# Kernel tuning notes

Measured on AMD Instinct MI355X. Metric: run time of the kernel, lower is better.

## Reference

```python
import jax, jax.numpy as jnp
import numpy as np

B, S, D, H = 4, 2048, 2048, 16
DH = D // H


def setup_inputs() -> dict:
    key = jax.random.key(0)
    ks = jax.random.split(key, 11)
    p = 0.02  # keep pre-softmax logits in a sane range
    return {
        "x": jax.random.normal(ks[0], (B, S, D), jnp.float32),
        "Wq": jax.random.normal(ks[1], (D, D), jnp.float32) * p,
        "bq": jax.random.normal(ks[2], (D,), jnp.float32) * p,
        "Wk": jax.random.normal(ks[3], (D, D), jnp.float32) * p,
        "bk": jax.random.normal(ks[4], (D,), jnp.float32) * p,
        "Wv": jax.random.normal(ks[5], (D, D), jnp.float32) * p,
        "bv": jax.random.normal(ks[6], (D,), jnp.float32) * p,
        "Wo": jax.random.normal(ks[7], (D, D), jnp.float32) * p,
        "bo": jax.random.normal(ks[8], (D,), jnp.float32) * p,
        "spiral_weight": jax.random.normal(ks[9], (H,), jnp.float32),
        "helix_rotation": jax.random.normal(ks[10], (D,), jnp.float32),
    }


def reference(x, Wq, bq, Wk, bk, Wv, bv, Wo, bo, spiral_weight, helix_rotation):
    b, s, d = x.shape
    h, dh = H, d // H
    # projections (torch Linear: x @ W.T + b), split into heads
    q = (x @ Wq.T + bq).reshape(b, s, h, dh)
    k = (x @ Wk.T + bk).reshape(b, s, h, dh)
    v = (x @ Wv.T + bv).reshape(b, s, h, dh)
    # cos/sin helix gating, applied per (head, head_dim) channel
    rot = helix_rotation.reshape(h, dh)
    q = q * jnp.cos(rot)
    k = k * jnp.sin(rot)
    # per-head scaled scores: [b,h,s,s]
    scores = jnp.einsum("bshd,bthd->bhst", q, k) / np.sqrt(dh).astype(np.float32)
    scores = scores * spiral_weight[None, :, None, None]
    attn = jax.nn.softmax(scores, axis=-1)
    out = jnp.einsum("bhst,bthd->bshd", attn, v).reshape(b, s, d)
    return out @ Wo.T + bo
```

## Files before the change

kernel.cpp:

```cpp
#include <hip/hip_runtime.h>
#include <math.h>

#define B_ 4
#define S_ 2048
#define D_ 2048
#define H_ 16
#define DH_ 128

typedef unsigned short u16;
typedef unsigned int u32;
typedef u16 u16x8 __attribute__((ext_vector_type(8)));
typedef __bf16 bf16x8 __attribute__((ext_vector_type(8)));
typedef float f32x4 __attribute__((ext_vector_type(4)));

__device__ inline u16 f2bf(float f) {
    unsigned int u = __builtin_bit_cast(unsigned int, f);
    unsigned int lsb = (u >> 16) & 1u;
    u += 0x7fffu + lsb;
    return (u16)(u >> 16);
}

__device__ inline f32x4 mfma16(u16x8 a, u16x8 b, f32x4 c) {
    return __builtin_amdgcn_mfma_f32_16x16x32_bf16(
        __builtin_bit_cast(bf16x8, a), __builtin_bit_cast(bf16x8, b), c, 0, 0, 0);
}

__device__ inline void gl2lds16(const u16* g, u16* l) {
    __builtin_amdgcn_global_load_lds(
        (const __attribute__((address_space(1))) void*)g,
        (__attribute__((address_space(3))) void*)l, 16, 0, 0);
}

__device__ inline void block_barrier() {
    asm volatile("" ::: "memory");
    __builtin_amdgcn_s_barrier();
    asm volatile("" ::: "memory");
}

__global__ __launch_bounds__(256) void cvt_f32_bf16(const float* __restrict__ src,
                                                    u16* __restrict__ dst, int n8) {
    int i = blockIdx.x * 256 + threadIdx.x;
    if (i >= n8) return;
    const float4* s = (const float4*)src + (size_t)i * 2;
    float4 a = s[0], b = s[1];
    u16x8 o;
    o[0] = f2bf(a.x); o[1] = f2bf(a.y); o[2] = f2bf(a.z); o[3] = f2bf(a.w);
    o[4] = f2bf(b.x); o[5] = f2bf(b.y); o[6] = f2bf(b.z); o[7] = f2bf(b.w);
    *((u16x8*)dst + i) = o;
}

__global__ __launch_bounds__(256) void cvt4_f32_bf16(const float* __restrict__ s0,
                                                     const float* __restrict__ s1,
                                                     const float* __restrict__ s2,
                                                     const float* __restrict__ s3,
                                                     u16* __restrict__ dst) {
    const int region = blockIdx.x >> 11;
    const int i = (blockIdx.x & 2047) * 256 + threadIdx.x;
    const float* src = region == 0 ? s0 : region == 1 ? s1 : region == 2 ? s2 : s3;
    const float4* s = (const float4*)src + (size_t)i * 2;
    float4 a = s[0], b = s[1];
    u16x8 o;
    o[0] = f2bf(a.x); o[1] = f2bf(a.y); o[2] = f2bf(a.z); o[3] = f2bf(a.w);
    o[4] = f2bf(b.x); o[5] = f2bf(b.y); o[6] = f2bf(b.z); o[7] = f2bf(b.w);
    *((u16x8*)dst + (size_t)region * 524288 + i) = o;
}

template <typename OutT>
__device__ __forceinline__ void gemm_core(const u16* __restrict__ A,
                                          const u16* __restrict__ Bw,
                                          const float* __restrict__ bias,
                                          const float* __restrict__ helix,
                                          OutT* __restrict__ C,
                                          int N, int K,
                                          int tm, int tn, int gate, int vout) {
    __shared__ __align__(16) u16 As[2][256 * 64];
    __shared__ __align__(16) u16 Bs[2][256 * 64];

    const int tid = threadIdx.x;
    const int lane = tid & 63, w = tid >> 6;
    const int lr = lane & 15, quad = lane >> 4;
    const int wm = w & 1, wn = w >> 1;
    const int NT = K >> 6;

    const u16* Asrc = A + (size_t)(tm * 256) * K;
    const u16* Bsrc = Bw + (size_t)(tn * 256) * K;

    u32 go[4][2];
    u32 lo[4][2];
#pragma unroll
    for (int q = 0; q < 2; ++q) {
        const int seg = w * 2 + q;
        const int i0 = seg * 8 + (lane >> 3);
        const int s0 = seg * 8;
        int row = (i0 & 63) | ((i0 >> 6) << 7);
        int rb = (s0 & 63) | ((s0 >> 6) << 7);
        go[0][q] = (u32)row * K + (((lane & 7) ^ (row & 7)) << 3);
        lo[0][q] = rb << 6;
        row += 64; rb += 64;
        go[3][q] = (u32)row * K + (((lane & 7) ^ (row & 7)) << 3);
        lo[3][q] = rb << 6;
        row = (i0 & 31) | ((i0 >> 5) << 6);
        rb = (s0 & 31) | ((s0 >> 5) << 6);
        go[1][q] = (u32)row * K + (((lane & 7) ^ (row & 7)) << 3);
        lo[1][q] = rb << 6;
        row += 32; rb += 32;
        go[2][q] = (u32)row * K + (((lane & 7) ^ (row & 7)) << 3);
        lo[2][q] = rb << 6;
    }

#define STAGE(u, tt)                                                          \
    do {                                                                      \
        const int kt_ = (((tt) < NT) ? (tt) : (NT - 1)) << 6;                 \
        const u16* gb_ = ((u) == 1 || (u) == 2) ? Bsrc : Asrc;                \
        u16* lb_ = ((u) == 1 || (u) == 2) ? Bs[(tt) & 1] : As[(tt) & 1];      \
        gl2lds16(gb_ + go[u][0] + kt_, lb_ + lo[u][0]);                       \
        gl2lds16(gb_ + go[u][1] + kt_, lb_ + lo[u][1]);                       \
    } while (0)

    const int koff0 = (quad * 8) ^ ((lr & 7) * 8);
    const int koff1 = (32 + quad * 8) ^ ((lr & 7) * 8);
    const int rA = wm * 128 + lr;
    const int rB = wn * 64 + lr;

    f32x4 zero = {0.f, 0.f, 0.f, 0.f};
    f32x4 acc[8][4];
#pragma unroll
    for (int im = 0; im < 8; ++im)
#pragma unroll
        for (int jn = 0; jn < 4; ++jn) acc[im][jn] = zero;

    u16x8 af[4][2], bf[4][2];

    STAGE(0, 0); STAGE(1, 0); STAGE(2, 0); STAGE(3, 0);
    STAGE(0, 1); STAGE(1, 1); STAGE(2, 1);
    asm volatile("s_waitcnt vmcnt(6)" ::: "memory");
    block_barrier();

    for (int t = 0; t < NT; ++t) {
        const u16* Ab = As[t & 1];
        const u16* Bb = Bs[t & 1];

#pragma unroll
        for (int im = 0; im < 4; ++im) {
            af[im][0] = *(const u16x8*)&Ab[(rA + im * 16) * 64 + koff0];
            af[im][1] = *(const u16x8*)&Ab[(rA + im * 16) * 64 + koff1];
        }
#pragma unroll
        for (int jn = 0; jn < 2; ++jn) {
            bf[jn][0] = *(const u16x8*)&Bb[(rB + jn * 16) * 64 + koff0];
            bf[jn][1] = *(const u16x8*)&Bb[(rB + jn * 16) * 64 + koff1];
        }
        STAGE(3, t + 1);
        block_barrier();
        asm volatile("s_waitcnt lgkmcnt(0)" ::: "memory");
        __builtin_amdgcn_s_setprio(1);
#pragma unroll
        for (int s = 0; s < 2; ++s)
#pragma unroll
            for (int im = 0; im < 4; ++im)
#pragma unroll
                for (int jn = 0; jn < 2; ++jn)
                    acc[im][jn] = mfma16(af[im][s], bf[jn][s], acc[im][jn]);
        __builtin_amdgcn_s_setprio(0);
        block_barrier();

#pragma unroll
        for (int jn = 2; jn < 4; ++jn) {
            bf[jn][0] = *(const u16x8*)&Bb[(rB + jn * 16) * 64 + koff0];
            bf[jn][1] = *(const u16x8*)&Bb[(rB + jn * 16) * 64 + koff1];
        }
        STAGE(0, t + 2);
        block_barrier();
        asm volatile("s_waitcnt lgkmcnt(0)" ::: "memory");
        __builtin_amdgcn_s_setprio(1);
#pragma unroll
        for (int s = 0; s < 2; ++s)
#pragma unroll
            for (int im = 0; im < 4; ++im)
#pragma unroll
                for (int jn = 2; jn < 4; ++jn)
                    acc[im][jn] = mfma16(af[im][s], bf[jn][s], acc[im][jn]);
        __builtin_amdgcn_s_setprio(0);
        block_barrier();

#pragma unroll
        for (int im = 0; im < 4; ++im) {
            af[im][0] = *(const u16x8*)&Ab[(rA + 64 + im * 16) * 64 + koff0];
            af[im][1] = *(const u16x8*)&Ab[(rA + 64 + im * 16) * 64 + koff1];
        }
        STAGE(1, t + 2);
        block_barrier();
        asm volatile("s_waitcnt lgkmcnt(0)" ::: "memory");
        __builtin_amdgcn_s_setprio(1);
#pragma unroll
        for (int s = 0; s < 2; ++s)
#pragma unroll
            for (int im = 0; im < 4; ++im)
#pragma unroll
                for (int jn = 0; jn < 2; ++jn)
                    acc[im + 4][jn] = mfma16(af[im][s], bf[jn][s], acc[im + 4][jn]);
        __builtin_amdgcn_s_setprio(0);
        block_barrier();

        STAGE(2, t + 2);
        asm volatile("s_waitcnt vmcnt(6)" ::: "memory");
        block_barrier();
        __builtin_amdgcn_s_setprio(1);
#pragma unroll
        for (int s = 0; s < 2; ++s)
#pragma unroll
            for (int im = 0; im < 4; ++im)
#pragma unroll
                for (int jn = 2; jn < 4; ++jn)
                    acc[im + 4][jn] = mfma16(af[im][s], bf[jn][s], acc[im + 4][jn]);
        __builtin_amdgcn_s_setprio(0);
        block_barrier();
    }
    asm volatile("s_waitcnt vmcnt(0)" ::: "memory");
#undef STAGE

    if (vout) {
#pragma unroll
        for (int im = 0; im < 8; ++im)
#pragma unroll
            for (int r = 0; r < 4; ++r) {
                int row = tm * 256 + wm * 128 + im * 16 + quad * 4 + r;
                float bs = bias[row];
#pragma unroll
                for (int jn = 0; jn < 4; ++jn) {
                    int col = tn * 256 + wn * 64 + jn * 16 + lr;
                    float val = acc[im][jn][r] + bs;
                    ((u16*)C)[(size_t)(col >> 11) * ((size_t)D_ * S_) +
                              (size_t)row * S_ + (col & (S_ - 1))] = f2bf(val);
                }
            }
    } else {
#pragma unroll
        for (int jn = 0; jn < 4; ++jn) {
            int col = tn * 256 + wn * 64 + jn * 16 + lr;
            float bs = bias[col];
            float g = 1.0f;
            if (gate == 1) g = cosf(helix[col]);
            if (gate == 2) g = sinf(helix[col]);
#pragma unroll
            for (int im = 0; im < 8; ++im)
#pragma unroll
                for (int r = 0; r < 4; ++r) {
                    int row = tm * 256 + wm * 128 + im * 16 + quad * 4 + r;
                    float val = (acc[im][jn][r] + bs) * g;
                    if constexpr (sizeof(OutT) == 2)
                        ((u16*)C)[(size_t)row * N + col] = f2bf(val);
                    else
                        ((float*)C)[(size_t)row * N + col] = val;
                }
        }
    }
}

template <typename OutT>
__global__ __launch_bounds__(512, 2) void gemm256(const u16* __restrict__ A,
                                                  const u16* __restrict__ Bw,
                                                  const float* __restrict__ bias,
                                                  const float* __restrict__ helix,
                                                  OutT* __restrict__ C,
                                                  int N, int K, int gate) {
    gemm_core<OutT>(A, Bw, bias, helix, C, N, K, blockIdx.y, blockIdx.x, gate, 0);
}

__global__ __launch_bounds__(512, 2) void gemm256_qkv(const u16* __restrict__ xbf,
                                                      const u16* __restrict__ Wq,
                                                      const u16* __restrict__ Wk,
                                                      const u16* __restrict__ Wv,
                                                      const float* __restrict__ bq,
                                                      const float* __restrict__ bk,
                                                      const float* __restrict__ bv,
                                                      const float* __restrict__ helix,
                                                      u16* __restrict__ Cq,
                                                      u16* __restrict__ Ck,
                                                      u16* __restrict__ Cv) {
    const int bid = blockIdx.x;
    const int region = bid >> 8;
    const int r = bid & 255;
    const u16* A;
    const u16* Bw;
    const float* bias;
    u16* C;
    int tm, tn, gate, vout;
    if (region == 0) {
        A = xbf; Bw = Wq; bias = bq; C = Cq;
        tn = r & 7; tm = r >> 3; gate = 1; vout = 0;
    } else if (region == 1) {
        A = xbf; Bw = Wk; bias = bk; C = Ck;
        tn = r & 7; tm = r >> 3; gate = 2; vout = 0;
    } else {
        A = Wv; Bw = xbf; bias = bv; C = Cv;
        tn = r & 31; tm = r >> 5; gate = 0; vout = 1;
    }
    gemm_core<u16>(A, Bw, bias, helix, C, D_, D_, tm, tn, gate, vout);
}

__global__ __launch_bounds__(256, 2) void helix_attn(const u16* __restrict__ Q,
                                                     const u16* __restrict__ Kq,
                                                     const u16* __restrict__ Vt,
                                                     const float* __restrict__ spiral,
                                                     u16* __restrict__ O) {
    __shared__ __align__(16) u16 Ks[64 * 128];
    __shared__ __align__(16) u16 Vs[128 * 64];
    __shared__ __align__(16) u16 Ps[128 * 64];

    const int tid = threadIdx.x;
    const int lane = tid & 63, w = tid >> 6;
    const int lr = lane & 15, quad = lane >> 4;

    const int bx = blockIdx.x;
    const int qt = bx & 15;
    const int h = (bx >> 4) & 15;
    const int b = bx >> 8;

    const size_t headoff = (size_t)b * S_ * D_ + (size_t)h * DH_;
    const u16* qp = Q + headoff;
    const u16* kp = Kq + headoff;
    const u16* vtp = Vt + ((size_t)b * H_ + h) * (size_t)DH_ * S_;

    const float scale2 = spiral[h] * 0.08838834764831845f * 1.4426950408889634f;

    u16x8 qf[2][4];
#pragma unroll
    for (int mb = 0; mb < 2; ++mb)
#pragma unroll
        for (int c = 0; c < 4; ++c) {
            u16x8 raw = *(const u16x8*)(qp + (size_t)(qt * 128 + mb * 64 + w * 16 + lr) * D_ +
                                        c * 32 + quad * 8);
#pragma unroll
            for (int j = 0; j < 8; ++j) {
                float f = __builtin_bit_cast(float, (u32)raw[j] << 16) * scale2;
                qf[mb][c][j] = f2bf(f);
            }
        }

    f32x4 zero = {0.f, 0.f, 0.f, 0.f};
    f32x4 Oacc[2][8];
#pragma unroll
    for (int mb = 0; mb < 2; ++mb)
#pragma unroll
        for (int n = 0; n < 8; ++n) Oacc[mb][n] = zero;
    float rs[2][4] = {{0.f, 0.f, 0.f, 0.f}, {0.f, 0.f, 0.f, 0.f}};

    const int rsw = (lr >> 1) & 7;
    const int wsw = (quad * 2) & 7;
    const int ksw = lr & 7;

    for (int tt = 0; tt < 32; ++tt) {
        const int t0 = tt * 64;
        __syncthreads();
#pragma unroll
        for (int p = 0; p < 4; ++p) {
            int lin = p * 256 + tid;
            int trow = lin >> 4;
            int kch = lin & 15;
            *(u16x8*)&Ks[trow * 128 + ((kch ^ (trow & 7)) * 8)] =
                *(const u16x8*)(kp + (size_t)(t0 + trow) * D_ + kch * 8);
            int drow = lin >> 3;
            int lc = lin & 7;
            *(u16x8*)&Vs[drow * 64 + ((lc ^ (drow & 7)) * 8)] =
                *(const u16x8*)(vtp + (size_t)drow * S_ + t0 + lc * 8);
        }
        __syncthreads();

        f32x4 Sacc[2][4] = {{zero, zero, zero, zero}, {zero, zero, zero, zero}};
#pragma unroll
        for (int c = 0; c < 4; ++c) {
#pragma unroll
            for (int j = 0; j < 4; ++j) {
                u16x8 kf = *(const u16x8*)&Ks[(j * 16 + lr) * 128 +
                                              (((c * 4 + quad) ^ ksw) * 8)];
                Sacc[0][j] = mfma16(qf[0][c], kf, Sacc[0][j]);
                Sacc[1][j] = mfma16(qf[1][c], kf, Sacc[1][j]);
            }
        }

#pragma unroll
        for (int mb = 0; mb < 2; ++mb)
#pragma unroll
            for (int j = 0; j < 4; ++j)
#pragma unroll
                for (int r = 0; r < 4; ++r) {
                    float p = exp2f(Sacc[mb][j][r]);
                    u32 u = __builtin_bit_cast(u32, p);
                    rs[mb][r] += __builtin_bit_cast(float, u & 0xffff0000u);
                    int prow = mb * 64 + w * 16 + quad * 4 + r;
                    int pchunk = (j * 2 + (lr >> 3)) ^ ((wsw + (r >> 1)) & 7);
                    Ps[prow * 64 + pchunk * 8 + (lr & 7)] = (u16)(u >> 16);
                }

#pragma unroll
        for (int ks = 0; ks < 2; ++ks) {
            int pch = ((ks * 4 + quad) ^ rsw) * 8;
            u16x8 pf0 = *(const u16x8*)&Ps[(w * 16 + lr) * 64 + pch];
            u16x8 pf1 = *(const u16x8*)&Ps[(64 + w * 16 + lr) * 64 + pch];
#pragma unroll
            for (int n = 0; n < 8; ++n) {
                u16x8 vf = *(const u16x8*)&Vs[(n * 16 + lr) * 64 +
                                              (((ks * 4 + quad) ^ ksw) * 8)];
                Oacc[0][n] = mfma16(pf0, vf, Oacc[0][n]);
                Oacc[1][n] = mfma16(pf1, vf, Oacc[1][n]);
            }
        }
    }

#pragma unroll
    for (int mb = 0; mb < 2; ++mb)
#pragma unroll
        for (int r = 0; r < 4; ++r) {
            float s = rs[mb][r];
#pragma unroll
            for (int off = 1; off < 16; off <<= 1) s += __shfl_xor(s, off, 64);
            float inv = 1.0f / s;
            int row = qt * 128 + mb * 64 + w * 16 + quad * 4 + r;
            u16* op = O + headoff + (size_t)row * D_;
#pragma unroll
            for (int n = 0; n < 8; ++n) op[n * 16 + lr] = f2bf(Oacc[mb][n][r] * inv);
        }
}

extern "C" void kernel_launch(void* const* d_in, const int* in_sizes, int n_in,
                              void* d_out, int out_size, void* d_ws, size_t ws_size,
                              hipStream_t stream) {
    const float* x = (const float*)d_in[0];
    const float* Wq = (const float*)d_in[1];
    const float* bq = (const float*)d_in[2];
    const float* Wk = (const float*)d_in[3];
    const float* bk = (const float*)d_in[4];
    const float* Wv = (const float*)d_in[5];
    const float* bv = (const float*)d_in[6];
    const float* Wo = (const float*)d_in[7];
    const float* bo = (const float*)d_in[8];
    const float* spiral = (const float*)d_in[9];
    const float* helix = (const float*)d_in[10];
    float* out = (float*)d_out;

    char* ws = (char*)d_ws;
    u16* xbf = (u16*)(ws);
    u16* wqb = (u16*)(ws + 33554432);
    u16* wkb = (u16*)(ws + 33554432 + 8388608);
    u16* wvb = (u16*)(ws + 33554432 + 16777216);
    u16* wob = (u16*)(ws + 33554432 + 25165824);
    u16* qb = (u16*)(ws + 67108864);
    u16* kb = (u16*)(ws + 67108864 + 33554432);
    u16* vtb = (u16*)(ws + 67108864 + 67108864);
    u16* attnb = xbf;

    const int NX = B_ * S_ * D_;

    cvt_f32_bf16<<<NX / 8 / 256, 256, 0, stream>>>(x, xbf, NX / 8);
    cvt4_f32_bf16<<<4 * 2048, 256, 0, stream>>>(Wq, Wk, Wv, Wo, wqb);

    gemm256_qkv<<<768, 512, 0, stream>>>(xbf, wqb, wkb, wvb, bq, bk, bv, helix,
                                         qb, kb, vtb);

    helix_attn<<<B_ * H_ * (S_ / 128), 256, 0, stream>>>(qb, kb, vtb, spiral, attnb);

    dim3 gq(D_ / 256, (B_ * S_) / 256);
    gemm256<float><<<gq, 512, 0, stream>>>(attnb, wob, bo, nullptr, out, D_, D_, 0);
}
```

Measured before the change: 691.1 us.

## Switch projection GEMM to 32x32x16 MFMA and pad attention V/P LDS tiles

The shared GEMM core now uses 32x32x16 bf16 MFMA tiles instead of 16x16x32. This halves the number of MFMA issues and changes fragment loads and the epilogue row mapping to match the 32x32 output layout. In the attention kernel, the Vs and Ps LDS buffers move from XOR swizzling to a padded row stride of 72, aiming to cut bank conflicts and address arithmetic. In exchange, the larger accumulator fragments may raise register pressure, the padded buffers use more LDS, and Ps keeps its XOR chunk index alongside the padding.

```diff
diff --git a/kernel.cpp b/kernel.cpp
--- a/kernel.cpp
+++ b/kernel.cpp
@@ -12,6 +12,7 @@
 typedef u16 u16x8 __attribute__((ext_vector_type(8)));
 typedef __bf16 bf16x8 __attribute__((ext_vector_type(8)));
 typedef float f32x4 __attribute__((ext_vector_type(4)));
+typedef float f32x16 __attribute__((ext_vector_type(16)));
 
 __device__ inline u16 f2bf(float f) {
     unsigned int u = __builtin_bit_cast(unsigned int, f);
@@ -22,6 +23,11 @@
 
 __device__ inline f32x4 mfma16(u16x8 a, u16x8 b, f32x4 c) {
     return __builtin_amdgcn_mfma_f32_16x16x32_bf16(
+        __builtin_bit_cast(bf16x8, a), __builtin_bit_cast(bf16x8, b), c, 0, 0, 0);
+}
+
+__device__ inline f32x16 mfma32(u16x8 a, u16x8 b, f32x16 c) {
+    return __builtin_amdgcn_mfma_f32_32x32x16_bf16(
         __builtin_bit_cast(bf16x8, a), __builtin_bit_cast(bf16x8, b), c, 0, 0, 0);
 }
 
@@ -78,7 +84,7 @@
 
     const int tid = threadIdx.x;
     const int lane = tid & 63, w = tid >> 6;
-    const int lr = lane & 15, quad = lane >> 4;
+    const int r32 = lane & 31, hi = lane >> 5;
     const int wm = w & 1, wn = w >> 1;
     const int NT = K >> 6;
 
@@ -117,19 +123,21 @@
         gl2lds16(gb_ + go[u][1] + kt_, lb_ + lo[u][1]);                       \
     } while (0)
 
-    const int koff0 = (quad * 8) ^ ((lr & 7) * 8);
-    const int koff1 = (32 + quad * 8) ^ ((lr & 7) * 8);
-    const int rA = wm * 128 + lr;
-    const int rB = wn * 64 + lr;
-
-    f32x4 zero = {0.f, 0.f, 0.f, 0.f};
-    f32x4 acc[8][4];
-#pragma unroll
-    for (int im = 0; im < 8; ++im)
-#pragma unroll
-        for (int jn = 0; jn < 4; ++jn) acc[im][jn] = zero;
-
-    u16x8 af[4][2], bf[4][2];
+    int kcs[4];
+#pragma unroll
+    for (int kk = 0; kk < 4; ++kk) kcs[kk] = (((kk * 2 + hi) ^ (r32 & 7)) * 8);
+    const int rA0 = (wm * 128 + r32) * 64;
+    const int rB0 = (wn * 64 + r32) * 64;
+
+    f32x16 acc[4][2];
+#pragma unroll
+    for (int mt = 0; mt < 4; ++mt)
+#pragma unroll
+        for (int nt = 0; nt < 2; ++nt)
+#pragma unroll
+            for (int e = 0; e < 16; ++e) acc[mt][nt][e] = 0.f;
+
+    u16x8 af[2][4], bf[2][4];
 
     STAGE(0, 0); STAGE(1, 0); STAGE(2, 0); STAGE(3, 0);
     STAGE(0, 1); STAGE(1, 1); STAGE(2, 1);
@@ -141,64 +149,64 @@
         const u16* Bb = Bs[t & 1];
 
 #pragma unroll
-        for (int im = 0; im < 4; ++im) {
-            af[im][0] = *(const u16x8*)&Ab[(rA + im * 16) * 64 + koff0];
-            af[im][1] = *(const u16x8*)&Ab[(rA + im * 16) * 64 + koff1];
-        }
-#pragma unroll
-        for (int jn = 0; jn < 2; ++jn) {
-            bf[jn][0] = *(const u16x8*)&Bb[(rB + jn * 16) * 64 + koff0];
-            bf[jn][1] = *(const u16x8*)&Bb[(rB + jn * 16) * 64 + koff1];
-        }
+        for (int mt = 0; mt < 2; ++mt)
+#pragma unroll
+            for (int kk = 0; kk < 4; ++kk)
+                af[mt][kk] = *(const u16x8*)&Ab[rA0 + mt * 2048 + kcs[kk]];
+#pragma unroll
+        for (int nt = 0; nt < 2; ++nt)
+#pragma unroll
+            for (int kk = 0; kk < 2; ++kk)
+                bf[nt][kk] = *(const u16x8*)&Bb[rB0 + nt * 2048 + kcs[kk]];
         STAGE(3, t + 1);
         block_barrier();
         asm volatile("s_waitcnt lgkmcnt(0)" ::: "memory");
         __builtin_amdgcn_s_setprio(1);
 #pragma unroll
-        for (int s = 0; s < 2; ++s)
-#pragma unroll
-            for (int im = 0; im < 4; ++im)
-#pragma unroll
-                for (int jn = 0; jn < 2; ++jn)
-                    acc[im][jn] = mfma16(af[im][s], bf[jn][s], acc[im][jn]);
+        for (int kk = 0; kk < 2; ++kk)
+#pragma unroll
+            for (int mt = 0; mt < 2; ++mt)
+#pragma unroll
+                for (int nt = 0; nt < 2; ++nt)
+                    acc[mt][nt] = mfma32(af[mt][kk], bf[nt][kk], acc[mt][nt]);
         __builtin_amdgcn_s_setprio(0);
         block_barrier();
 
 #pragma unroll
-        for (int jn = 2; jn < 4; ++jn) {
-            bf[jn][0] = *(const u16x8*)&Bb[(rB + jn * 16) * 64 + koff0];
-            bf[jn][1] = *(const u16x8*)&Bb[(rB + jn * 16) * 64 + koff1];
-        }
+        for (int nt = 0; nt < 2; ++nt)
+#pragma unroll
+            for (int kk = 2; kk < 4; ++kk)
+                bf[nt][kk] = *(const u16x8*)&Bb[rB0 + nt * 2048 + kcs[kk]];
         STAGE(0, t + 2);
         block_barrier();
         asm volatile("s_waitcnt lgkmcnt(0)" ::: "memory");
         __builtin_amdgcn_s_setprio(1);
 #pragma unroll
-        for (int s = 0; s < 2; ++s)
-#pragma unroll
-            for (int im = 0; im < 4; ++im)
-#pragma unroll
-                for (int jn = 2; jn < 4; ++jn)
-                    acc[im][jn] = mfma16(af[im][s], bf[jn][s], acc[im][jn]);
+        for (int kk = 2; kk < 4; ++kk)
+#pragma unroll
+            for (int mt = 0; mt < 2; ++mt)
+#pragma unroll
+                for (int nt = 0; nt < 2; ++nt)
+                    acc[mt][nt] = mfma32(af[mt][kk], bf[nt][kk], acc[mt][nt]);
         __builtin_amdgcn_s_setprio(0);
         block_barrier();
 
 #pragma unroll
-        for (int im = 0; im < 4; ++im) {
-            af[im][0] = *(const u16x8*)&Ab[(rA + 64 + im * 16) * 64 + koff0];
-            af[im][1] = *(const u16x8*)&Ab[(rA + 64 + im * 16) * 64 + koff1];
-        }
+        for (int mt = 0; mt < 2; ++mt)
+#pragma unroll
+            for (int kk = 0; kk < 4; ++kk)
+                af[mt][kk] = *(const u16x8*)&Ab[rA0 + (2 + mt) * 2048 + kcs[kk]];
         STAGE(1, t + 2);
         block_barrier();
         asm volatile("s_waitcnt lgkmcnt(0)" ::: "memory");
         __builtin_amdgcn_s_setprio(1);
 #pragma unroll
-        for (int s = 0; s < 2; ++s)
-#pragma unroll
-            for (int im = 0; im < 4; ++im)
-#pragma unroll
-                for (int jn = 0; jn < 2; ++jn)
-                    acc[im + 4][jn] = mfma16(af[im][s], bf[jn][s], acc[im + 4][jn]);
+        for (int kk = 0; kk < 2; ++kk)
+#pragma unroll
+            for (int mt = 0; mt < 2; ++mt)
+#pragma unroll
+                for (int nt = 0; nt < 2; ++nt)
+                    acc[2 + mt][nt] = mfma32(af[mt][kk], bf[nt][kk], acc[2 + mt][nt]);
         __builtin_amdgcn_s_setprio(0);
         block_barrier();
 
@@ -207,12 +215,12 @@
         block_barrier();
         __builtin_amdgcn_s_setprio(1);
 #pragma unroll
-        for (int s = 0; s < 2; ++s)
-#pragma unroll
-            for (int im = 0; im < 4; ++im)
-#pragma unroll
-                for (int jn = 2; jn < 4; ++jn)
-                    acc[im + 4][jn] = mfma16(af[im][s], bf[jn][s], acc[im + 4][jn]);
+        for (int kk = 2; kk < 4; ++kk)
+#pragma unroll
+            for (int mt = 0; mt < 2; ++mt)
+#pragma unroll
+                for (int nt = 0; nt < 2; ++nt)
+                    acc[2 + mt][nt] = mfma32(af[mt][kk], bf[nt][kk], acc[2 + mt][nt]);
         __builtin_amdgcn_s_setprio(0);
         block_barrier();
     }
@@ -221,33 +229,33 @@
 
     if (vout) {
 #pragma unroll
-        for (int im = 0; im < 8; ++im)
-#pragma unroll
-            for (int r = 0; r < 4; ++r) {
-                int row = tm * 256 + wm * 128 + im * 16 + quad * 4 + r;
+        for (int mt = 0; mt < 4; ++mt)
+#pragma unroll
+            for (int reg = 0; reg < 16; ++reg) {
+                int row = tm * 256 + wm * 128 + mt * 32 + (reg & 3) + 8 * (reg >> 2) + 4 * hi;
                 float bs = bias[row];
 #pragma unroll
-                for (int jn = 0; jn < 4; ++jn) {
-                    int col = tn * 256 + wn * 64 + jn * 16 + lr;
-                    float val = acc[im][jn][r] + bs;
+                for (int nt = 0; nt < 2; ++nt) {
+                    int col = tn * 256 + wn * 64 + nt * 32 + r32;
+                    float val = acc[mt][nt][reg] + bs;
                     ((u16*)C)[(size_t)(col >> 11) * ((size_t)D_ * S_) +
                               (size_t)row * S_ + (col & (S_ - 1))] = f2bf(val);
                 }
             }
     } else {
 #pragma unroll
-        for (int jn = 0; jn < 4; ++jn) {
-            int col = tn * 256 + wn * 64 + jn * 16 + lr;
+        for (int nt = 0; nt < 2; ++nt) {
+            int col = tn * 256 + wn * 64 + nt * 32 + r32;
             float bs = bias[col];
             float g = 1.0f;
             if (gate == 1) g = cosf(helix[col]);
             if (gate == 2) g = sinf(helix[col]);
 #pragma unroll
-            for (int im = 0; im < 8; ++im)
-#pragma unroll
-                for (int r = 0; r < 4; ++r) {
-                    int row = tm * 256 + wm * 128 + im * 16 + quad * 4 + r;
-                    float val = (acc[im][jn][r] + bs) * g;
+            for (int mt = 0; mt < 4; ++mt)
+#pragma unroll
+                for (int reg = 0; reg < 16; ++reg) {
+                    int row = tm * 256 + wm * 128 + mt * 32 + (reg & 3) + 8 * (reg >> 2) + 4 * hi;
+                    float val = (acc[mt][nt][reg] + bs) * g;
                     if constexpr (sizeof(OutT) == 2)
                         ((u16*)C)[(size_t)row * N + col] = f2bf(val);
                     else
@@ -305,8 +313,8 @@
                                                      const float* __restrict__ spiral,
                                                      u16* __restrict__ O) {
     __shared__ __align__(16) u16 Ks[64 * 128];
-    __shared__ __align__(16) u16 Vs[128 * 64];
-    __shared__ __align__(16) u16 Ps[128 * 64];
+    __shared__ __align__(16) u16 Vs[128 * 72];
+    __shared__ __align__(16) u16 Ps[128 * 72];
 
     const int tid = threadIdx.x;
     const int lane = tid & 63, w = tid >> 6;
@@ -361,9 +369,9 @@
             *(u16x8*)&Ks[trow * 128 + ((kch ^ (trow & 7)) * 8)] =
                 *(const u16x8*)(kp + (size_t)(t0 + trow) * D_ + kch * 8);
             int drow = lin >> 3;
-            int lc = lin & 7;
-            *(u16x8*)&Vs[drow * 64 + ((lc ^ (drow & 7)) * 8)] =
-                *(const u16x8*)(vtp + (size_t)drow * S_ + t0 + lc * 8);
+            int tch = (lin & 7) * 8;
+            *(u16x8*)&Vs[drow * 72 + tch] =
+                *(const u16x8*)(vtp + (size_t)drow * S_ + t0 + tch);
         }
         __syncthreads();
 
@@ -390,18 +398,17 @@
                     rs[mb][r] += __builtin_bit_cast(float, u & 0xffff0000u);
                     int prow = mb * 64 + w * 16 + quad * 4 + r;
                     int pchunk = (j * 2 + (lr >> 3)) ^ ((wsw + (r >> 1)) & 7);
-                    Ps[prow * 64 + pchunk * 8 + (lr & 7)] = (u16)(u >> 16);
+                    Ps[prow * 72 + pchunk * 8 + (lr & 7)] = (u16)(u >> 16);
                 }
 
 #pragma unroll
         for (int ks = 0; ks < 2; ++ks) {
             int pch = ((ks * 4 + quad) ^ rsw) * 8;
-            u16x8 pf0 = *(const u16x8*)&Ps[(w * 16 + lr) * 64 + pch];
-            u16x8 pf1 = *(const u16x8*)&Ps[(64 + w * 16 + lr) * 64 + pch];
+            u16x8 pf0 = *(const u16x8*)&Ps[(w * 16 + lr) * 72 + pch];
+            u16x8 pf1 = *(const u16x8*)&Ps[(64 + w * 16 + lr) * 72 + pch];
 #pragma unroll
             for (int n = 0; n < 8; ++n) {
-                u16x8 vf = *(const u16x8*)&Vs[(n * 16 + lr) * 64 +
-                                              (((ks * 4 + quad) ^ ksw) * 8)];
+                u16x8 vf = *(const u16x8*)&Vs[(n * 16 + lr) * 72 + ks * 32 + quad * 8];
                 Oacc[0][n] = mfma16(pf0, vf, Oacc[0][n]);
                 Oacc[1][n] = mfma16(pf1, vf, Oacc[1][n]);
             }
```

After: 691.4 us. About the same (+0.0%).

## Remap GEMM block order for XCD locality and pad attention V/P LDS tiles

Applied to the files above, without the earlier changes.

Both GEMM kernels now permute the linear block index so that consecutive hardware-dispatched blocks (round-robined over 8 XCDs) land on tiles that share operands within one XCD's L2. The V-projection tile mapping is also transposed. In the attention kernel, the V and P shared-memory tiles switch from an XOR swizzle to a row pitch padded from 64 to 72 elements, which simplifies address math. The padding uses more LDS and may change the bank-conflict pattern.

```diff
diff --git a/kernel.cpp b/kernel.cpp
--- a/kernel.cpp
+++ b/kernel.cpp
@@ -257,14 +257,12 @@
     }
 }
 
-template <typename OutT>
-__global__ __launch_bounds__(512, 2) void gemm256(const u16* __restrict__ A,
-                                                  const u16* __restrict__ Bw,
-                                                  const float* __restrict__ bias,
-                                                  const float* __restrict__ helix,
-                                                  OutT* __restrict__ C,
-                                                  int N, int K, int gate) {
-    gemm_core<OutT>(A, Bw, bias, helix, C, N, K, blockIdx.y, blockIdx.x, gate, 0);
+__global__ __launch_bounds__(512, 2) void gemm256_o(const u16* __restrict__ A,
+                                                    const u16* __restrict__ Bw,
+                                                    const float* __restrict__ bias,
+                                                    float* __restrict__ C) {
+    const int L = (blockIdx.x & 7) * 32 + (blockIdx.x >> 3);
+    gemm_core<float>(A, Bw, bias, nullptr, C, D_, D_, L >> 3, L & 7, 0, 0);
 }
 
 __global__ __launch_bounds__(512, 2) void gemm256_qkv(const u16* __restrict__ xbf,
@@ -278,9 +276,9 @@
                                                       u16* __restrict__ Cq,
                                                       u16* __restrict__ Ck,
                                                       u16* __restrict__ Cv) {
-    const int bid = blockIdx.x;
-    const int region = bid >> 8;
-    const int r = bid & 255;
+    const int L = (blockIdx.x & 7) * 96 + (blockIdx.x >> 3);
+    const int region = L >> 8;
+    const int r = L & 255;
     const u16* A;
     const u16* Bw;
     const float* bias;
@@ -294,7 +292,7 @@
         tn = r & 7; tm = r >> 3; gate = 2; vout = 0;
     } else {
         A = Wv; Bw = xbf; bias = bv; C = Cv;
-        tn = r & 31; tm = r >> 5; gate = 0; vout = 1;
+        tn = r >> 3; tm = r & 7; gate = 0; vout = 1;
     }
     gemm_core<u16>(A, Bw, bias, helix, C, D_, D_, tm, tn, gate, vout);
 }
@@ -305,8 +303,8 @@
                                                      const float* __restrict__ spiral,
                                                      u16* __restrict__ O) {
     __shared__ __align__(16) u16 Ks[64 * 128];
-    __shared__ __align__(16) u16 Vs[128 * 64];
-    __shared__ __align__(16) u16 Ps[128 * 64];
+    __shared__ __align__(16) u16 Vs[128 * 72];
+    __shared__ __align__(16) u16 Ps[128 * 72];
 
     const int tid = threadIdx.x;
     const int lane = tid & 63, w = tid >> 6;
@@ -361,9 +359,9 @@
             *(u16x8*)&Ks[trow * 128 + ((kch ^ (trow & 7)) * 8)] =
                 *(const u16x8*)(kp + (size_t)(t0 + trow) * D_ + kch * 8);
             int drow = lin >> 3;
-            int lc = lin & 7;
-            *(u16x8*)&Vs[drow * 64 + ((lc ^ (drow & 7)) * 8)] =
-                *(const u16x8*)(vtp + (size_t)drow * S_ + t0 + lc * 8);
+            int tch = (lin & 7) * 8;
+            *(u16x8*)&Vs[drow * 72 + tch] =
+                *(const u16x8*)(vtp + (size_t)drow * S_ + t0 + tch);
         }
         __syncthreads();
 
@@ -390,18 +388,17 @@
                     rs[mb][r] += __builtin_bit_cast(float, u & 0xffff0000u);
                     int prow = mb * 64 + w * 16 + quad * 4 + r;
                     int pchunk = (j * 2 + (lr >> 3)) ^ ((wsw + (r >> 1)) & 7);
-                    Ps[prow * 64 + pchunk * 8 + (lr & 7)] = (u16)(u >> 16);
+                    Ps[prow * 72 + pchunk * 8 + (lr & 7)] = (u16)(u >> 16);
                 }
 
 #pragma unroll
         for (int ks = 0; ks < 2; ++ks) {
             int pch = ((ks * 4 + quad) ^ rsw) * 8;
-            u16x8 pf0 = *(const u16x8*)&Ps[(w * 16 + lr) * 64 + pch];
-            u16x8 pf1 = *(const u16x8*)&Ps[(64 + w * 16 + lr) * 64 + pch];
+            u16x8 pf0 = *(const u16x8*)&Ps[(w * 16 + lr) * 72 + pch];
+            u16x8 pf1 = *(const u16x8*)&Ps[(64 + w * 16 + lr) * 72 + pch];
 #pragma unroll
             for (int n = 0; n < 8; ++n) {
-                u16x8 vf = *(const u16x8*)&Vs[(n * 16 + lr) * 64 +
-                                              (((ks * 4 + quad) ^ ksw) * 8)];
+                u16x8 vf = *(const u16x8*)&Vs[(n * 16 + lr) * 72 + ks * 32 + quad * 8];
                 Oacc[0][n] = mfma16(pf0, vf, Oacc[0][n]);
                 Oacc[1][n] = mfma16(pf1, vf, Oacc[1][n]);
             }
@@ -460,6 +457,5 @@
 
     helix_attn<<<B_ * H_ * (S_ / 128), 256, 0, stream>>>(qb, kb, vtb, spiral, attnb);
 
-    dim3 gq(D_ / 256, (B_ * S_) / 256);
-    gemm256<float><<<gq, 512, 0, stream>>>(attnb, wob, bo, nullptr, out, D_, D_, 0);
-}
+    gemm256_o<<<256, 512, 0, stream>>>(attnb, wob, bo, out);
+}
```

After: 643.3 us. 1.07x faster.
